# Kernel tuning notes

Hardware: AMD Instinct MI355X
Metric: run time of the kernel (lower is better)

Reference implementation:

```python
import jax, jax.numpy as jnp
import numpy as np

BS, SEQ, DIM, DIM_MLP, E = 2, 2048, 1024, 4096, 8
STD = 0.02  # nn.init.normal_(weight, std=0.02)


def setup_inputs() -> dict:
    key = jax.random.key(0)
    k_x, k_idx, k_w1, k_w2 = jax.random.split(key, 4)
    x = jax.random.normal(k_x, (BS, SEQ, DIM), dtype=jnp.float32)
    expert_idx = jax.random.randint(k_idx, (BS, SEQ), 0, E, dtype=jnp.int32)
    W1 = jax.random.normal(k_w1, (E, DIM, DIM_MLP), dtype=jnp.float32) * STD
    b1 = jnp.zeros((E, DIM_MLP), dtype=jnp.float32)
    W2 = jax.random.normal(k_w2, (E, DIM_MLP, DIM), dtype=jnp.float32) * STD
    b2 = jnp.zeros((E, DIM), dtype=jnp.float32)
    return {"x": x, "expert_idx": expert_idx, "W1": W1, "b1": b1, "W2": W2, "b2": b2}


def reference(x, expert_idx, W1, b1, W2, b2):
    # Compute ALL experts on all tokens (faithful to the torch module).
    # h: [bs, seq, E, dim_mlp]
    h = jnp.einsum("bsd,edm->bsem", x, W1) + b1
    h = jax.nn.gelu(h, approximate=False)  # torch nn.GELU default = exact erf
    # feat: [bs, seq, E, dim]  (== torch.cat along feature dim, reshaped)
    feat = jnp.einsum("bsem,emd->bsed", h, W2) + b2
    # Per-token gather of the assigned expert's output (top-1 select).
    idx = expert_idx.astype(jnp.int32)[:, :, None, None]  # [bs, seq, 1, 1]
    out = jnp.take_along_axis(feat, idx, axis=2)[:, :, 0, :]  # [bs, seq, dim]
    return out
```

## Files before the change

### kernel.cpp

```cpp
#include <hip/hip_runtime.h>
#include <hip/hip_bf16.h>
#include <math.h>

#define TOK   4096
#define DIM   1024
#define DMLP  4096
#define NE    8
#define BM    128
#define BN    128
#define BN2   64
#define BK    128
#define PADMAX (TOK + NE * BM)
#define NTILES (PADMAX / BM)

typedef __attribute__((ext_vector_type(8))) short  short8;
typedef __attribute__((ext_vector_type(4))) float  float4v;
typedef __attribute__((ext_vector_type(4))) unsigned short ushort4v;
typedef __attribute__((ext_vector_type(2))) unsigned long long ull2;

#define ASYNC16(gp, lp) __builtin_amdgcn_global_load_lds( \
    (const __attribute__((address_space(1))) unsigned int*)(gp), \
    (__attribute__((address_space(3))) unsigned int*)(lp), 16, 0, 0)

#define SWZ(R, C) (((C) & 8) | (((C) ^ (R)) & 7))
#define FRAG_OFF(R, C) ((((R) << 4) + SWZ(R, C)) << 3)

static __device__ __forceinline__ unsigned short f2bf(float f) {
  unsigned u = __float_as_uint(f);
  u += 0x7fffu + ((u >> 16) & 1u);
  return (unsigned short)(u >> 16);
}

static __device__ __forceinline__ float gelu_erf(float v) {
  const float x = fabsf(v) * 0.70710678118654752f;
  const float t = __builtin_amdgcn_rcpf(1.0f + 0.3275911f * x);
  const float poly = ((((1.061405429f * t - 1.453152027f) * t + 1.421413741f) * t
                       - 0.284496736f) * t + 0.254829592f) * t;
  const float erf_abs = 1.0f - poly * __expf(-x * x);
  return 0.5f * v * (1.0f + copysignf(erf_abs, v));
}

__global__ void group_kernel(const int* __restrict__ eidx,
                             int* __restrict__ perm,
                             int* __restrict__ tile_e) {
  __shared__ int cnt[NE], off[NE], len[NE], cur[NE];
  const int tid = threadIdx.x;
  if (tid < NE) cnt[tid] = 0;
  __syncthreads();
  for (int i = tid; i < TOK; i += 256) atomicAdd(&cnt[eidx[i]], 1);
  __syncthreads();
  if (tid == 0) {
    int o = 0;
    for (int e = 0; e < NE; e++) {
      off[e] = o;
      len[e] = ((cnt[e] + BM - 1) / BM) * BM;
      cur[e] = o;
      o += len[e];
    }
  }
  __syncthreads();
  for (int s = tid; s < PADMAX; s += 256) perm[s] = -1;
  __syncthreads();
  for (int i = tid; i < TOK; i += 256) {
    const int e = eidx[i];
    const int p = atomicAdd(&cur[e], 1);
    perm[p] = i;
  }
  __syncthreads();
  for (int t = tid; t < NTILES; t += 256) {
    const int row = t * BM;
    int te = -1;
    for (int e = 0; e < NE; e++)
      if (row >= off[e] && row < off[e] + len[e]) te = e;
    tile_e[t] = te;
  }
}

__global__ __launch_bounds__(256)
void convtrans_kernel(const float* __restrict__ W, unsigned short* __restrict__ WT,
                      int K, int N) {
  __shared__ unsigned short T[64][68];
  const int e  = blockIdx.z;
  const int k0 = blockIdx.y * 64, n0 = blockIdx.x * 64;
  const float* Win = W + (size_t)e * K * N;
  unsigned short* Wout = WT + (size_t)e * K * N;
  const int tid = threadIdx.x;
  const int i4 = tid & 15;
  const int kq = (tid >> 4) * 4;
  float4v v[4];
#pragma unroll
  for (int j = 0; j < 4; j++)
    v[j] = *(const float4v*)(Win + (size_t)(k0 + kq + j) * N + n0 + i4 * 4);
#pragma unroll
  for (int q = 0; q < 4; q++) {
    ushort4v w;
#pragma unroll
    for (int j = 0; j < 4; j++) w[j] = f2bf(v[j][q]);
    *(ushort4v*)&T[i4 * 4 + q][kq] = w;
  }
  __syncthreads();
  const int g  = tid & 7;
  const int nb = tid >> 3;
#pragma unroll
  for (int r = 0; r < 2; r++) {
    const int n = nb + 32 * r;
    const unsigned long long v0 = *(const unsigned long long*)&T[n][g * 8];
    const unsigned long long v1 = *(const unsigned long long*)&T[n][g * 8 + 4];
    ull2 o; o[0] = v0; o[1] = v1;
    *(ull2*)&Wout[(size_t)(n0 + n) * K + k0 + g * 8] = o;
  }
}

__global__ __launch_bounds__(256)
void xgather_kernel(const float* __restrict__ x, const int* __restrict__ perm,
                    unsigned short* __restrict__ xg) {
  const int slot = blockIdx.x;
  const int t    = perm[slot];
  const int tid  = threadIdx.x;
  ushort4v o = (ushort4v){0, 0, 0, 0};
  if (t >= 0) {
    const float4v v = *(const float4v*)(x + (size_t)t * DIM + tid * 4);
#pragma unroll
    for (int q = 0; q < 4; q++) o[q] = f2bf(v[q]);
  }
  *(ushort4v*)(xg + (size_t)slot * DIM + tid * 4) = o;
}

__global__ __launch_bounds__(256)
void gemm1_kernel(const unsigned short* __restrict__ xg,
                  const unsigned short* __restrict__ W1T,
                  const float* __restrict__ b1, const int* __restrict__ tile_e,
                  unsigned short* __restrict__ h) {
  const int bt = blockIdx.y;
  const int te = tile_e[bt];
  if (te < 0) return;
  const int n0 = blockIdx.x * BN;
  const unsigned short* Asrc = xg + (size_t)bt * BM * DIM;
  const unsigned short* Bsrc = W1T + (size_t)te * DIM * DMLP + (size_t)n0 * DIM;
  const int tid = threadIdx.x;

  __shared__ __align__(16) unsigned short SMEM[2 * BM * BK];

  const int rr = tid >> 4, q = tid & 15;
  const int cs = SWZ(rr, q);
  const unsigned short* a0 = Asrc + (size_t)rr * DIM + cs * 8;
  const unsigned short* b0 = Bsrc + (size_t)rr * DIM + cs * 8;

  const int wid = tid >> 6, lane = tid & 63;
  const int wm = (wid >> 1) * 64, wn = (wid & 1) * 64;
  const int l15 = lane & 15, quad = lane >> 4;

  float4v acc[4][4];
#pragma unroll
  for (int i = 0; i < 4; i++)
#pragma unroll
    for (int j = 0; j < 4; j++) acc[i][j] = (float4v){0.f, 0.f, 0.f, 0.f};

  for (int k0 = 0; k0 < DIM; k0 += BK) {
#pragma unroll
    for (int t = 0; t < 8; t++)
      ASYNC16(a0 + (size_t)(16 * t) * DIM + k0, &SMEM[(t * 256 + tid) * 8]);
#pragma unroll
    for (int t = 0; t < 8; t++)
      ASYNC16(b0 + (size_t)(16 * t) * DIM + k0, &SMEM[BM * BK + (t * 256 + tid) * 8]);
    __syncthreads();

#pragma unroll
    for (int hh = 0; hh < 4; hh++) {
      short8 a[4], b[4];
      const int C = hh * 4 + quad;
#pragma unroll
      for (int i = 0; i < 4; i++)
        a[i] = *(const short8*)&SMEM[FRAG_OFF(wm + i * 16 + l15, C)];
#pragma unroll
      for (int j = 0; j < 4; j++)
        b[j] = *(const short8*)&SMEM[BM * BK + FRAG_OFF(wn + j * 16 + l15, C)];
#pragma unroll
      for (int i = 0; i < 4; i++)
#pragma unroll
        for (int j = 0; j < 4; j++)
          acc[i][j] = __builtin_amdgcn_mfma_f32_16x16x32_bf16(a[i], b[j], acc[i][j], 0, 0, 0);
    }
    __syncthreads();
  }

#pragma unroll
  for (int i = 0; i < 4; i++) {
#pragma unroll
    for (int j = 0; j < 4; j++) {
      const int colL = wn + j * 16 + l15;
      const float bias = b1[te * DMLP + n0 + colL];
#pragma unroll
      for (int r = 0; r < 4; r++) {
        const int rowL = wm + i * 16 + quad * 4 + r;
        SMEM[rowL * BN + colL] = f2bf(gelu_erf(acc[i][j][r] + bias));
      }
    }
  }
  __syncthreads();
  const int gg = tid & 15;
  const int rb = tid >> 4;
#pragma unroll
  for (int p = 0; p < 8; p++) {
    const int rowL = rb + p * 16;
    const ull2 v = *(const ull2*)&SMEM[rowL * BN + gg * 8];
    *(ull2*)&h[(size_t)(bt * BM + rowL) * DMLP + n0 + gg * 8] = v;
  }
}

__global__ __launch_bounds__(256)
void gemm2_kernel(const unsigned short* __restrict__ h,
                  const unsigned short* __restrict__ W2T,
                  const float* __restrict__ b2, const int* __restrict__ perm,
                  const int* __restrict__ tile_e, float* __restrict__ out) {
  const int bt = blockIdx.y;
  const int te = tile_e[bt];
  if (te < 0) return;
  const int n0 = blockIdx.x * BN2;
  const unsigned short* Asrc = h + (size_t)bt * BM * DMLP;
  const unsigned short* Bsrc = W2T + (size_t)te * DMLP * DIM + (size_t)n0 * DMLP;
  const int tid = threadIdx.x;

  __shared__ __align__(16) unsigned short As[BM * BK];
  __shared__ __align__(16) unsigned short Bs[BN2 * BK];

  const int rr = tid >> 4, q = tid & 15;
  const int cs = SWZ(rr, q);
  const unsigned short* a0 = Asrc + (size_t)rr * DMLP + cs * 8;
  const unsigned short* b0 = Bsrc + (size_t)rr * DMLP + cs * 8;

  const int wid = tid >> 6, lane = tid & 63;
  const int wm = (wid >> 1) * 64, wn = (wid & 1) * 32;
  const int l15 = lane & 15, quad = lane >> 4;

  float4v acc[4][2];
#pragma unroll
  for (int i = 0; i < 4; i++)
#pragma unroll
    for (int j = 0; j < 2; j++) acc[i][j] = (float4v){0.f, 0.f, 0.f, 0.f};

  for (int k0 = 0; k0 < DMLP; k0 += BK) {
#pragma unroll
    for (int t = 0; t < 8; t++)
      ASYNC16(a0 + (size_t)(16 * t) * DMLP + k0, &As[(t * 256 + tid) * 8]);
#pragma unroll
    for (int t = 0; t < 4; t++)
      ASYNC16(b0 + (size_t)(16 * t) * DMLP + k0, &Bs[(t * 256 + tid) * 8]);
    __syncthreads();

#pragma unroll
    for (int hh = 0; hh < 4; hh++) {
      short8 a[4], b[2];
      const int C = hh * 4 + quad;
#pragma unroll
      for (int i = 0; i < 4; i++) a[i] = *(const short8*)&As[FRAG_OFF(wm + i * 16 + l15, C)];
#pragma unroll
      for (int j = 0; j < 2; j++) b[j] = *(const short8*)&Bs[FRAG_OFF(wn + j * 16 + l15, C)];
#pragma unroll
      for (int i = 0; i < 4; i++)
#pragma unroll
        for (int j = 0; j < 2; j++)
          acc[i][j] = __builtin_amdgcn_mfma_f32_16x16x32_bf16(a[i], b[j], acc[i][j], 0, 0, 0);
    }
    __syncthreads();
  }

#pragma unroll
  for (int i = 0; i < 4; i++) {
#pragma unroll
    for (int j = 0; j < 2; j++) {
      const int col = n0 + wn + j * 16 + l15;
      const float bias = b2[te * DIM + col];
#pragma unroll
      for (int r = 0; r < 4; r++) {
        const int row  = wm + i * 16 + quad * 4 + r;
        const int slot = bt * BM + row;
        const int t    = perm[slot];
        if (t >= 0) out[(size_t)t * DIM + col] = acc[i][j][r] + bias;
      }
    }
  }
}

extern "C" void kernel_launch(void* const* d_in, const int* in_sizes, int n_in,
                              void* d_out, int out_size, void* d_ws, size_t ws_size,
                              hipStream_t stream) {
  const float* x    = (const float*)d_in[0];
  const int*   eidx = (const int*)d_in[1];
  const float* W1   = (const float*)d_in[2];
  const float* b1   = (const float*)d_in[3];
  const float* W2   = (const float*)d_in[4];
  const float* b2   = (const float*)d_in[5];
  float* out = (float*)d_out;

  char* ws = (char*)d_ws;
  int* perm   = (int*)ws;
  int* tile_e = (int*)(ws + PADMAX * sizeof(int));
  unsigned short* xg  = (unsigned short*)(ws + 32768);
  unsigned short* h   = (unsigned short*)(ws + 32768 + 10485760);
  unsigned short* W1T = (unsigned short*)(ws + 32768 + 10485760 + 41943040);
  unsigned short* W2T = (unsigned short*)((char*)W1T + 67108864);

  group_kernel<<<1, 256, 0, stream>>>(eidx, perm, tile_e);
  convtrans_kernel<<<dim3(DMLP / 64, DIM / 64, NE), 256, 0, stream>>>(W1, W1T, DIM, DMLP);
  convtrans_kernel<<<dim3(DIM / 64, DMLP / 64, NE), 256, 0, stream>>>(W2, W2T, DMLP, DIM);
  xgather_kernel<<<PADMAX, 256, 0, stream>>>(x, perm, xg);
  gemm1_kernel<<<dim3(DMLP / BN, NTILES), 256, 0, stream>>>(xg, W1T, b1, tile_e, h);
  gemm2_kernel<<<dim3(DIM / BN2, NTILES), 256, 0, stream>>>(h, W2T, b2, perm, tile_e, out);
}
```

Measured before the change: 469.0 us.

## Pair same-expert row tiles in gemm2 and merge prep kernels into one launch

Gemm2 now processes two 128-row tiles belonging to the same expert per block (256 rows by 64 columns), so each W2 tile loaded into LDS is reused across twice as many rows. Each wave computes a 64x64 output block instead of 64x32, which raises the MFMA-to-load ratio. The group kernel builds the list of paired tiles. Separately, the two weight convert-transpose launches and the x gather are fused into a single prep kernel to cut launch overhead. In exchange, gemm2 uses more LDS and more accumulator registers per block and launches fewer blocks, which may lower occupancy and parallelism.

```diff
diff --git a/kernel.cpp b/kernel.cpp
--- a/kernel.cpp
+++ b/kernel.cpp
@@ -12,6 +12,7 @@
 #define BK    128
 #define PADMAX (TOK + NE * BM)
 #define NTILES (PADMAX / BM)
+#define MAXSUP 24
 
 typedef __attribute__((ext_vector_type(8))) short  short8;
 typedef __attribute__((ext_vector_type(4))) float  float4v;
@@ -42,7 +43,10 @@
 
 __global__ void group_kernel(const int* __restrict__ eidx,
                              int* __restrict__ perm,
-                             int* __restrict__ tile_e) {
+                             int* __restrict__ tile_e,
+                             int* __restrict__ supA,
+                             int* __restrict__ supB,
+                             int* __restrict__ supE) {
   __shared__ int cnt[NE], off[NE], len[NE], cur[NE];
   const int tid = threadIdx.x;
   if (tid < NE) cnt[tid] = 0;
@@ -57,6 +61,18 @@
       cur[e] = o;
       o += len[e];
     }
+    int ns = 0;
+    for (int e = 0; e < NE; e++) {
+      const int nt = len[e] / BM;
+      for (int p = 0; p < nt; p += 2) {
+        const int pb = (p + 1 < nt) ? (p + 1) : p;
+        supA[ns] = off[e] + p * BM;
+        supB[ns] = off[e] + pb * BM;
+        supE[ns] = e;
+        ns++;
+      }
+    }
+    for (; ns < MAXSUP; ns++) { supA[ns] = 0; supB[ns] = 0; supE[ns] = -1; }
   }
   __syncthreads();
   for (int s = tid; s < PADMAX; s += 256) perm[s] = -1;
@@ -76,15 +92,13 @@
   }
 }
 
-__global__ __launch_bounds__(256)
-void convtrans_kernel(const float* __restrict__ W, unsigned short* __restrict__ WT,
-                      int K, int N) {
-  __shared__ unsigned short T[64][68];
-  const int e  = blockIdx.z;
-  const int k0 = blockIdx.y * 64, n0 = blockIdx.x * 64;
+static __device__ __forceinline__
+void conv_body(const float* __restrict__ W, unsigned short* __restrict__ WT,
+               int K, int N, int bx, int by, int e, int tid,
+               unsigned short T[64][68]) {
+  const int k0 = by * 64, n0 = bx * 64;
   const float* Win = W + (size_t)e * K * N;
   unsigned short* Wout = WT + (size_t)e * K * N;
-  const int tid = threadIdx.x;
   const int i4 = tid & 15;
   const int kq = (tid >> 4) * 4;
   float4v v[4];
@@ -112,18 +126,29 @@
 }
 
 __global__ __launch_bounds__(256)
-void xgather_kernel(const float* __restrict__ x, const int* __restrict__ perm,
-                    unsigned short* __restrict__ xg) {
-  const int slot = blockIdx.x;
-  const int t    = perm[slot];
-  const int tid  = threadIdx.x;
-  ushort4v o = (ushort4v){0, 0, 0, 0};
-  if (t >= 0) {
-    const float4v v = *(const float4v*)(x + (size_t)t * DIM + tid * 4);
-#pragma unroll
-    for (int q = 0; q < 4; q++) o[q] = f2bf(v[q]);
-  }
-  *(ushort4v*)(xg + (size_t)slot * DIM + tid * 4) = o;
+void prep_kernel(const float* __restrict__ W1, unsigned short* __restrict__ W1T,
+                 const float* __restrict__ W2, unsigned short* __restrict__ W2T,
+                 const float* __restrict__ x, const int* __restrict__ perm,
+                 unsigned short* __restrict__ xg) {
+  __shared__ unsigned short T[64][68];
+  const int bid = blockIdx.x;
+  const int tid = threadIdx.x;
+  if (bid < 8192) {
+    conv_body(W1, W1T, DIM, DMLP, bid & 63, (bid >> 6) & 15, bid >> 10, tid, T);
+  } else if (bid < 16384) {
+    const int b = bid - 8192;
+    conv_body(W2, W2T, DMLP, DIM, b & 15, (b >> 4) & 63, b >> 10, tid, T);
+  } else {
+    const int slot = bid - 16384;
+    const int t    = perm[slot];
+    ushort4v o = (ushort4v){0, 0, 0, 0};
+    if (t >= 0) {
+      const float4v v = *(const float4v*)(x + (size_t)t * DIM + tid * 4);
+#pragma unroll
+      for (int q = 0; q < 4; q++) o[q] = f2bf(v[q]);
+    }
+    *(ushort4v*)(xg + (size_t)slot * DIM + tid * 4) = o;
+  }
 }
 
 __global__ __launch_bounds__(256)
@@ -212,37 +237,42 @@
 void gemm2_kernel(const unsigned short* __restrict__ h,
                   const unsigned short* __restrict__ W2T,
                   const float* __restrict__ b2, const int* __restrict__ perm,
-                  const int* __restrict__ tile_e, float* __restrict__ out) {
-  const int bt = blockIdx.y;
-  const int te = tile_e[bt];
+                  const int* __restrict__ supA, const int* __restrict__ supB,
+                  const int* __restrict__ supE, float* __restrict__ out) {
+  const int s  = blockIdx.y;
+  const int te = supE[s];
   if (te < 0) return;
+  const int rowA = supA[s], rowB = supB[s];
   const int n0 = blockIdx.x * BN2;
-  const unsigned short* Asrc = h + (size_t)bt * BM * DMLP;
-  const unsigned short* Bsrc = W2T + (size_t)te * DMLP * DIM + (size_t)n0 * DMLP;
   const int tid = threadIdx.x;
 
-  __shared__ __align__(16) unsigned short As[BM * BK];
+  __shared__ __align__(16) unsigned short As[256 * BK];
   __shared__ __align__(16) unsigned short Bs[BN2 * BK];
 
   const int rr = tid >> 4, q = tid & 15;
   const int cs = SWZ(rr, q);
-  const unsigned short* a0 = Asrc + (size_t)rr * DMLP + cs * 8;
-  const unsigned short* b0 = Bsrc + (size_t)rr * DMLP + cs * 8;
+  const unsigned short* aA = h + (size_t)(rowA + rr) * DMLP + cs * 8;
+  const unsigned short* aB = h + (size_t)(rowB + rr) * DMLP + cs * 8;
+  const unsigned short* b0 = W2T + (size_t)te * DMLP * DIM
+                           + (size_t)(n0 + rr) * DMLP + cs * 8;
 
   const int wid = tid >> 6, lane = tid & 63;
-  const int wm = (wid >> 1) * 64, wn = (wid & 1) * 32;
+  const int wm = wid * 64;
   const int l15 = lane & 15, quad = lane >> 4;
 
-  float4v acc[4][2];
+  float4v acc[4][4];
 #pragma unroll
   for (int i = 0; i < 4; i++)
 #pragma unroll
-    for (int j = 0; j < 2; j++) acc[i][j] = (float4v){0.f, 0.f, 0.f, 0.f};
+    for (int j = 0; j < 4; j++) acc[i][j] = (float4v){0.f, 0.f, 0.f, 0.f};
 
   for (int k0 = 0; k0 < DMLP; k0 += BK) {
 #pragma unroll
     for (int t = 0; t < 8; t++)
-      ASYNC16(a0 + (size_t)(16 * t) * DMLP + k0, &As[(t * 256 + tid) * 8]);
+      ASYNC16(aA + (size_t)(16 * t) * DMLP + k0, &As[(t * 256 + tid) * 8]);
+#pragma unroll
+    for (int t = 0; t < 8; t++)
+      ASYNC16(aB + (size_t)(16 * t) * DMLP + k0, &As[((t + 8) * 256 + tid) * 8]);
 #pragma unroll
     for (int t = 0; t < 4; t++)
       ASYNC16(b0 + (size_t)(16 * t) * DMLP + k0, &Bs[(t * 256 + tid) * 8]);
@@ -250,31 +280,33 @@
 
 #pragma unroll
     for (int hh = 0; hh < 4; hh++) {
-      short8 a[4], b[2];
+      short8 a[4], b[4];
       const int C = hh * 4 + quad;
 #pragma unroll
-      for (int i = 0; i < 4; i++) a[i] = *(const short8*)&As[FRAG_OFF(wm + i * 16 + l15, C)];
-#pragma unroll
-      for (int j = 0; j < 2; j++) b[j] = *(const short8*)&Bs[FRAG_OFF(wn + j * 16 + l15, C)];
-#pragma unroll
       for (int i = 0; i < 4; i++)
-#pragma unroll
-        for (int j = 0; j < 2; j++)
+        a[i] = *(const short8*)&As[FRAG_OFF(wm + i * 16 + l15, C)];
+#pragma unroll
+      for (int j = 0; j < 4; j++)
+        b[j] = *(const short8*)&Bs[FRAG_OFF(j * 16 + l15, C)];
+#pragma unroll
+      for (int i = 0; i < 4; i++)
+#pragma unroll
+        for (int j = 0; j < 4; j++)
           acc[i][j] = __builtin_amdgcn_mfma_f32_16x16x32_bf16(a[i], b[j], acc[i][j], 0, 0, 0);
     }
     __syncthreads();
   }
 
+  const int halfbase = (wm < 128) ? (rowA + wm) : (rowB + (wm - 128));
 #pragma unroll
   for (int i = 0; i < 4; i++) {
 #pragma unroll
-    for (int j = 0; j < 2; j++) {
-      const int col = n0 + wn + j * 16 + l15;
+    for (int j = 0; j < 4; j++) {
+      const int col = n0 + j * 16 + l15;
       const float bias = b2[te * DIM + col];
 #pragma unroll
       for (int r = 0; r < 4; r++) {
-        const int row  = wm + i * 16 + quad * 4 + r;
-        const int slot = bt * BM + row;
+        const int slot = halfbase + i * 16 + quad * 4 + r;
         const int t    = perm[slot];
         if (t >= 0) out[(size_t)t * DIM + col] = acc[i][j][r] + bias;
       }
@@ -296,15 +328,16 @@
   char* ws = (char*)d_ws;
   int* perm   = (int*)ws;
   int* tile_e = (int*)(ws + PADMAX * sizeof(int));
+  int* supA   = (int*)(ws + 20736);
+  int* supB   = (int*)(ws + 20832);
+  int* supE   = (int*)(ws + 20928);
   unsigned short* xg  = (unsigned short*)(ws + 32768);
   unsigned short* h   = (unsigned short*)(ws + 32768 + 10485760);
   unsigned short* W1T = (unsigned short*)(ws + 32768 + 10485760 + 41943040);
   unsigned short* W2T = (unsigned short*)((char*)W1T + 67108864);
 
-  group_kernel<<<1, 256, 0, stream>>>(eidx, perm, tile_e);
-  convtrans_kernel<<<dim3(DMLP / 64, DIM / 64, NE), 256, 0, stream>>>(W1, W1T, DIM, DMLP);
-  convtrans_kernel<<<dim3(DIM / 64, DMLP / 64, NE), 256, 0, stream>>>(W2, W2T, DMLP, DIM);
-  xgather_kernel<<<PADMAX, 256, 0, stream>>>(x, perm, xg);
+  group_kernel<<<1, 256, 0, stream>>>(eidx, perm, tile_e, supA, supB, supE);
+  prep_kernel<<<16384 + PADMAX, 256, 0, stream>>>(W1, W1T, W2, W2T, x, perm, xg);
   gemm1_kernel<<<dim3(DMLP / BN, NTILES), 256, 0, stream>>>(xg, W1T, b1, tile_e, h);
-  gemm2_kernel<<<dim3(DIM / BN2, NTILES), 256, 0, stream>>>(h, W2T, b2, perm, tile_e, out);
-}
+  gemm2_kernel<<<dim3(DIM / BN2, MAXSUP), 256, 0, stream>>>(h, W2T, b2, perm, supA, supB, supE, out);
+}
```

Result: no change. 475.0 us (+1.3%).
